# Optimization experiments

Measured on AMD Instinct MI355X. Metric: run time of the kernel, lower is better.

The kernel has to match this reference:

```python
import jax, jax.numpy as jnp
import numpy as np

OUT_FEATURES = 11008
IN_FEATURES = 4096
BLOCK_SIZE = 128
NUM_BLOCKS = IN_FEATURES // BLOCK_SIZE  # 32
M_TOKENS = 4096  # flattened batch*seq


def _pack_int4(q):
    # q: int8 values in [-8, 7], flattened; pack 2 nibbles per int8 (matches pack_int4_to_int8)
    flat = q.reshape(-1)
    u = (flat.astype(jnp.int32) + 8).astype(jnp.uint8)
    packed = (u[0::2] | (u[1::2] << 4)).astype(jnp.int8)
    return packed


def _unpack_int4(packed, shape):
    # matches unpack_int8_to_int4
    pu = packed.astype(jnp.uint8)
    lower = pu & 15
    upper = (pu >> 4) & 15
    un = jnp.stack([lower, upper], axis=1).reshape(-1)
    n = int(np.prod(shape))
    un = un[:n].astype(jnp.int8) - 8
    return un.reshape(shape)


def setup_inputs() -> dict:
    key = jax.random.key(0)
    k_x, k_w, k_b = jax.random.split(key, 3)
    x = jax.random.normal(k_x, (M_TOKENS, IN_FEATURES), dtype=jnp.float32)
    w = jax.random.normal(k_w, (OUT_FEATURES, IN_FEATURES), dtype=jnp.float32) * 0.02
    bias = jax.random.normal(k_b, (OUT_FEATURES,), dtype=jnp.float32) * 0.01
    # blockwise symmetric 4-bit quantization (matches _quantize_blockwise)
    wr = w.reshape(OUT_FEATURES, NUM_BLOCKS, BLOCK_SIZE).transpose(1, 2, 0)  # (nb, bs, out)
    max_val = jnp.max(jnp.abs(wr), axis=1, keepdims=True)  # (nb, 1, out)
    qmax = 7.0
    scale3 = jnp.clip(max_val / qmax, 1e-8, None)
    q = jnp.clip(jnp.round(wr / scale3), -8, 7).astype(jnp.int8)  # (nb, bs, out)
    scale = scale3.squeeze(1)  # (nb, out)
    packed_w = _pack_int4(q)
    return {"x": x, "packed_w": packed_w, "scale": scale, "bias": bias}


def reference(x, packed_w, scale, bias):
    # unpack int4 nibbles -> (num_blocks, block_size, out)
    q = _unpack_int4(packed_w, (NUM_BLOCKS, BLOCK_SIZE, OUT_FEATURES))
    # dequantize with per-(block, out-channel) scale
    w_deq = q.astype(jnp.float32) * scale[:, None, :]  # (nb, bs, out)
    # y = x @ W^T + b, with x blocked along the in dimension
    xb = x.reshape(x.shape[0], NUM_BLOCKS, BLOCK_SIZE)
    y = jnp.einsum('mnb,nbo->mo', xb, w_deq) + bias
    return y
```

## Files before the change

kernel.cpp:

```cpp
#include <hip/hip_runtime.h>
#include <hip/hip_bf16.h>
#include <stdint.h>

#define NOUT 11008
#define KIN  4096
#define MTOK 4096
#define PLD  5504
#define NSTEP 128
#define NTN 43
#define NTM 16
#define ACHUNK 16384
#define BCHUNK 16384
#define WSA_BYTES ((size_t)NTM * NSTEP * ACHUNK)
#define WSW_BYTES ((size_t)NTN * NSTEP * BCHUNK)

typedef short bf16x8 __attribute__((ext_vector_type(8)));
typedef float f32x4  __attribute__((ext_vector_type(4)));

typedef __attribute__((address_space(3))) uint8_t lds_u8_t;
typedef __attribute__((address_space(1))) const uint8_t glb_u8_t;

__device__ __forceinline__ uint32_t bfpack(float lo, float hi){
    __hip_bfloat16 a = __float2bfloat16(lo);
    __hip_bfloat16 b = __float2bfloat16(hi);
    uint16_t ua, ub;
    __builtin_memcpy(&ua, &a, 2);
    __builtin_memcpy(&ub, &b, 2);
    return (uint32_t)ua | ((uint32_t)ub << 16);
}

__device__ __forceinline__ int swzA(int r){ return ((r >> 1) & 3) << 4; }

__device__ __forceinline__ int imin(int a, int b){ return a < b ? a : b; }

__global__ __launch_bounds__(256)
void prepA(const float* __restrict__ x, uint8_t* __restrict__ wsA)
{
    int gid = blockIdx.x * 256 + threadIdx.x;
    int m  = gid >> 10;
    int k  = (gid & 1023) << 2;
    float4 v = *reinterpret_cast<const float4*>(x + (size_t)m * KIN + k);
    uint32_t lo = bfpack(v.x, v.y), hi = bfpack(v.z, v.w);
    int mt = m >> 8, ml = m & 255, t = k >> 5, kl = k & 31;
    size_t dst = (size_t)(mt * NSTEP + t) * ACHUNK + ml * 64 + ((kl * 2) ^ swzA(ml));
    *reinterpret_cast<uint2*>(wsA + dst) = make_uint2(lo, hi);
}

__global__ __launch_bounds__(256)
void prepW2(const int32_t* __restrict__ pw, const float* __restrict__ sc,
            uint8_t* __restrict__ wsW)
{
    const int t  = blockIdx.x;
    const int nt = blockIdx.y;
    const int c  = threadIdx.x;
    const int col = nt * 256 + c;
    const int np  = col >> 1;
    const uint32_t sh = (uint32_t)(col & 1) * 4;
    const int32_t* p = pw + (size_t)(t * 32) * PLD + np;
    const float s  = sc[(size_t)(t >> 2) * NOUT + col];
    const float m8 = -8.f * s;
    uint8_t* out = wsW + ((size_t)nt * NSTEP + t) * BCHUNK + c * 64;
#pragma unroll
    for (int k8 = 0; k8 < 4; ++k8) {
        uint32_t r[4];
#pragma unroll
        for (int kk = 0; kk < 4; ++kk) {
            uint32_t w0 = (uint32_t)p[(size_t)(k8 * 8 + kk * 2)     * PLD];
            uint32_t w1 = (uint32_t)p[(size_t)(k8 * 8 + kk * 2 + 1) * PLD];
            float f0 = fmaf((float)((w0 >> sh) & 15u), s, m8);
            float f1 = fmaf((float)((w1 >> sh) & 15u), s, m8);
            r[kk] = bfpack(f0, f1);
        }
        *reinterpret_cast<uint4*>(out + ((k8 * 16) ^ swzA(c))) = *reinterpret_cast<uint4*>(r);
    }
}

__global__ __launch_bounds__(512, 1)
void qlin_gemm14(const uint8_t* __restrict__ wsA, const uint8_t* __restrict__ wsW,
                 const float* __restrict__ bias, float* __restrict__ y)
{
    __shared__ __align__(16) uint8_t ldsA[4][ACHUNK];

    const int tid  = threadIdx.x;
    const int lane = tid & 63;
    const int wid  = tid >> 6;
    const int wr = wid >> 2, wc = wid & 3;

    const int lb = (blockIdx.x & 7) * 86 + (blockIdx.x >> 3);
    const int mt = lb / NTN, nt = lb % NTN;
    const int m0 = mt * 256, n0 = nt * 256;

    const int cl = lane & 15;
    const int k8 = lane >> 4;

    int aOff[8];
#pragma unroll
    for (int i = 0; i < 8; ++i) {
        int ml = wr * 128 + i * 16 + cl;
        aOff[i] = ml * 64 + ((k8 * 16) ^ swzA(ml));
    }
    int bOff[4];
#pragma unroll
    for (int j = 0; j < 4; ++j) {
        int cc = wc * 64 + j * 16 + cl;
        bOff[j] = cc * 64 + ((k8 * 16) ^ swzA(cc));
    }

    const uint8_t* wsAbase = wsA + (size_t)mt * NSTEP * ACHUNK;
    const uint8_t* wsWbase = wsW + (size_t)nt * NSTEP * BCHUNK;

    f32x4 acc[8][4];
#pragma unroll
    for (int i = 0; i < 8; ++i)
#pragma unroll
        for (int j = 0; j < 4; ++j)
            acc[i][j] = (f32x4){0.f, 0.f, 0.f, 0.f};

    bf16x8 af[4], BFa[4], BFb[4];

#define STAGE_A(buf, t) do { \
    const uint8_t* g_ = wsAbase + (size_t)(t) * ACHUNK + tid * 16; \
    __builtin_amdgcn_global_load_lds((glb_u8_t*)(g_),        (lds_u8_t*)(&ldsA[buf][tid*16]),        16, 0, 0); \
    __builtin_amdgcn_global_load_lds((glb_u8_t*)(g_ + 8192), (lds_u8_t*)(&ldsA[buf][tid*16 + 8192]), 16, 0, 0); \
} while(0)

#define LOADB(BF, tn) do { \
    const uint8_t* gb_ = wsWbase + (size_t)(tn) * BCHUNK; \
    _Pragma("unroll") \
    for (int j = 0; j < 4; ++j) BF[j] = *reinterpret_cast<const bf16x8*>(gb_ + bOff[j]); \
} while(0)

#define BAR() do { \
    asm volatile("" ::: "memory"); \
    __builtin_amdgcn_s_barrier(); \
    asm volatile("" ::: "memory"); \
} while(0)

#define PH_O(cb, sb, st, BFC, BFN, tn) do { \
    STAGE_A(sb, st); \
    LOADB(BFN, tn); \
    _Pragma("unroll") \
    for (int i = 0; i < 4; ++i) af[i] = *reinterpret_cast<const bf16x8*>(ldsA[cb] + aOff[i]); \
    BAR(); \
    __builtin_amdgcn_s_setprio(1); \
    _Pragma("unroll") \
    for (int j = 0; j < 4; ++j) { _Pragma("unroll") \
        for (int i = 0; i < 4; ++i) \
            acc[i][j] = __builtin_amdgcn_mfma_f32_16x16x32_bf16(af[i], BFC[j], acc[i][j], 0, 0, 0); } \
    __builtin_amdgcn_s_setprio(0); \
    BAR(); \
} while(0)

#define PH_E(cb, BFC) do { \
    _Pragma("unroll") \
    for (int i = 0; i < 4; ++i) af[i] = *reinterpret_cast<const bf16x8*>(ldsA[cb] + aOff[4 + i]); \
    BAR(); \
    __builtin_amdgcn_s_setprio(1); \
    _Pragma("unroll") \
    for (int j = 0; j < 4; ++j) { _Pragma("unroll") \
        for (int i = 0; i < 4; ++i) \
            acc[4 + i][j] = __builtin_amdgcn_mfma_f32_16x16x32_bf16(af[i], BFC[j], acc[4 + i][j], 0, 0, 0); } \
    __builtin_amdgcn_s_setprio(0); \
    asm volatile("s_waitcnt vmcnt(12)" ::: "memory"); \
    __builtin_amdgcn_sched_barrier(0); \
    BAR(); \
} while(0)

    STAGE_A(0, 0);
    STAGE_A(1, 1);
    STAGE_A(2, 2);
    LOADB(BFa, 0);
    asm volatile("s_waitcnt vmcnt(8)" ::: "memory");
    __builtin_amdgcn_sched_barrier(0);
    BAR();

#pragma unroll 1
    for (int tb = 0; tb < NSTEP; tb += 4) {
        { const int st = imin(tb + 3, 127), tn = imin(tb + 1, 127);
          PH_O(0, 3, st, BFa, BFb, tn);  PH_E(0, BFa); }
        { const int st = imin(tb + 4, 127), tn = imin(tb + 2, 127);
          PH_O(1, 0, st, BFb, BFa, tn);  PH_E(1, BFb); }
        { const int st = imin(tb + 5, 127), tn = imin(tb + 3, 127);
          PH_O(2, 1, st, BFa, BFb, tn);  PH_E(2, BFa); }
        { const int st = imin(tb + 6, 127), tn = imin(tb + 4, 127);
          PH_O(3, 2, st, BFb, BFa, tn);  PH_E(3, BFb); }
    }

    float bv[4];
#pragma unroll
    for (int j = 0; j < 4; ++j) bv[j] = bias[n0 + wc * 64 + j * 16 + cl];
    const int rg = (lane >> 4) * 4;
#pragma unroll
    for (int i = 0; i < 8; ++i) {
        const int mrow = m0 + wr * 128 + i * 16 + rg;
#pragma unroll
        for (int r = 0; r < 4; ++r) {
            float* yp = y + (size_t)(mrow + r) * NOUT + n0 + wc * 64 + cl;
#pragma unroll
            for (int j = 0; j < 4; ++j)
                yp[j * 16] = acc[i][j][r] + bv[j];
        }
    }

#undef STAGE_A
#undef LOADB
#undef BAR
#undef PH_O
#undef PH_E
}

extern "C" void kernel_launch(void* const* d_in, const int* in_sizes, int n_in,
                              void* d_out, int out_size, void* d_ws, size_t ws_size,
                              hipStream_t stream)
{
    const float*   xin  = (const float*)d_in[0];
    const int32_t* pw   = (const int32_t*)d_in[1];
    const float*   scal = (const float*)d_in[2];
    const float*   bias = (const float*)d_in[3];
    float* y = (float*)d_out;

    uint8_t* wsA = (uint8_t*)d_ws;
    uint8_t* wsW = wsA + WSA_BYTES;

    prepA<<<dim3((MTOK * (KIN / 4)) / 256), 256, 0, stream>>>(xin, wsA);
    prepW2<<<dim3(NSTEP, NTN), 256, 0, stream>>>(pw, scal, wsW);
    qlin_gemm14<<<dim3(NTM * NTN), 512, 0, stream>>>(wsA, wsW, bias, y);
}
```

Measured before the change: 477.9 us.

## Double K-step depth and stage B tiles through LDS instead of direct global loads

Each pipeline step now covers 64 K elements (32 KB chunks) instead of 32, halving the number of steps and barriers. The weight tile is now staged into LDS through asynchronous global_load_lds double-buffering, where before each wave loaded B fragments straight from global memory into registers. The prep kernels change their workspace layouts to match. The intent is to cut barrier and step overhead and to hide B-load latency. In exchange, LDS use rises to 160 KB and the pipeline moves to triple-buffered A with a new waitcnt schedule, which risks stalls or occupancy limits.

```diff
diff --git a/kernel.cpp b/kernel.cpp
--- a/kernel.cpp
+++ b/kernel.cpp
@@ -6,13 +6,13 @@
 #define KIN  4096
 #define MTOK 4096
 #define PLD  5504
-#define NSTEP 128
+#define NSTEP 64
 #define NTN 43
 #define NTM 16
-#define ACHUNK 16384
-#define BCHUNK 16384
-#define WSA_BYTES ((size_t)NTM * NSTEP * ACHUNK)
-#define WSW_BYTES ((size_t)NTN * NSTEP * BCHUNK)
+#define ACH 32768
+#define BCH 32768
+#define WSA_BYTES ((size_t)NTM * NSTEP * ACH)
+#define WSW_BYTES ((size_t)NTN * NSTEP * BCH)
 
 typedef short bf16x8 __attribute__((ext_vector_type(8)));
 typedef float f32x4  __attribute__((ext_vector_type(4)));
@@ -31,8 +31,6 @@
 
 __device__ __forceinline__ int swzA(int r){ return ((r >> 1) & 3) << 4; }
 
-__device__ __forceinline__ int imin(int a, int b){ return a < b ? a : b; }
-
 __global__ __launch_bounds__(256)
 void prepA(const float* __restrict__ x, uint8_t* __restrict__ wsA)
 {
@@ -41,8 +39,8 @@
     int k  = (gid & 1023) << 2;
     float4 v = *reinterpret_cast<const float4*>(x + (size_t)m * KIN + k);
     uint32_t lo = bfpack(v.x, v.y), hi = bfpack(v.z, v.w);
-    int mt = m >> 8, ml = m & 255, t = k >> 5, kl = k & 31;
-    size_t dst = (size_t)(mt * NSTEP + t) * ACHUNK + ml * 64 + ((kl * 2) ^ swzA(ml));
+    int mt = m >> 8, ml = m & 255, t = k >> 6, kh = (k >> 5) & 1, kl = k & 31;
+    size_t dst = (size_t)(mt * NSTEP + t) * ACH + ml * 128 + kh * 64 + ((kl * 2) ^ swzA(ml));
     *reinterpret_cast<uint2*>(wsA + dst) = make_uint2(lo, hi);
 }
 
@@ -56,12 +54,12 @@
     const int col = nt * 256 + c;
     const int np  = col >> 1;
     const uint32_t sh = (uint32_t)(col & 1) * 4;
-    const int32_t* p = pw + (size_t)(t * 32) * PLD + np;
-    const float s  = sc[(size_t)(t >> 2) * NOUT + col];
+    const int32_t* p = pw + (size_t)(t * 64) * PLD + np;
+    const float s  = sc[(size_t)(t >> 1) * NOUT + col];
     const float m8 = -8.f * s;
-    uint8_t* out = wsW + ((size_t)nt * NSTEP + t) * BCHUNK + c * 64;
-#pragma unroll
-    for (int k8 = 0; k8 < 4; ++k8) {
+    uint8_t* out = wsW + ((size_t)nt * NSTEP + t) * BCH + c * 128;
+#pragma unroll
+    for (int k8 = 0; k8 < 8; ++k8) {
         uint32_t r[4];
 #pragma unroll
         for (int kk = 0; kk < 4; ++kk) {
@@ -71,15 +69,17 @@
             float f1 = fmaf((float)((w1 >> sh) & 15u), s, m8);
             r[kk] = bfpack(f0, f1);
         }
-        *reinterpret_cast<uint4*>(out + ((k8 * 16) ^ swzA(c))) = *reinterpret_cast<uint4*>(r);
+        *reinterpret_cast<uint4*>(out + (k8 >> 2) * 64 + (((k8 & 3) * 16) ^ swzA(c)))
+            = *reinterpret_cast<uint4*>(r);
     }
 }
 
 __global__ __launch_bounds__(512, 1)
-void qlin_gemm14(const uint8_t* __restrict__ wsA, const uint8_t* __restrict__ wsW,
+void qlin_gemm15(const uint8_t* __restrict__ wsA, const uint8_t* __restrict__ wsW,
                  const float* __restrict__ bias, float* __restrict__ y)
 {
-    __shared__ __align__(16) uint8_t ldsA[4][ACHUNK];
+    __shared__ __align__(16) uint8_t ldsA[3][ACH];
+    __shared__ __align__(16) uint8_t ldsB[2][BCH];
 
     const int tid  = threadIdx.x;
     const int lane = tid & 63;
@@ -97,17 +97,17 @@
 #pragma unroll
     for (int i = 0; i < 8; ++i) {
         int ml = wr * 128 + i * 16 + cl;
-        aOff[i] = ml * 64 + ((k8 * 16) ^ swzA(ml));
+        aOff[i] = ml * 128 + ((k8 * 16) ^ swzA(ml));
     }
     int bOff[4];
 #pragma unroll
     for (int j = 0; j < 4; ++j) {
         int cc = wc * 64 + j * 16 + cl;
-        bOff[j] = cc * 64 + ((k8 * 16) ^ swzA(cc));
-    }
-
-    const uint8_t* wsAbase = wsA + (size_t)mt * NSTEP * ACHUNK;
-    const uint8_t* wsWbase = wsW + (size_t)nt * NSTEP * BCHUNK;
+        bOff[j] = cc * 128 + ((k8 * 16) ^ swzA(cc));
+    }
+
+    const uint8_t* wsAbase = wsA + (size_t)mt * NSTEP * ACH;
+    const uint8_t* wsWbase = wsW + (size_t)nt * NSTEP * BCH;
 
     f32x4 acc[8][4];
 #pragma unroll
@@ -116,18 +116,22 @@
         for (int j = 0; j < 4; ++j)
             acc[i][j] = (f32x4){0.f, 0.f, 0.f, 0.f};
 
-    bf16x8 af[4], BFa[4], BFb[4];
+    bf16x8 af[4], bf2[4][2];
 
 #define STAGE_A(buf, t) do { \
-    const uint8_t* g_ = wsAbase + (size_t)(t) * ACHUNK + tid * 16; \
-    __builtin_amdgcn_global_load_lds((glb_u8_t*)(g_),        (lds_u8_t*)(&ldsA[buf][tid*16]),        16, 0, 0); \
-    __builtin_amdgcn_global_load_lds((glb_u8_t*)(g_ + 8192), (lds_u8_t*)(&ldsA[buf][tid*16 + 8192]), 16, 0, 0); \
-} while(0)
-
-#define LOADB(BF, tn) do { \
-    const uint8_t* gb_ = wsWbase + (size_t)(tn) * BCHUNK; \
-    _Pragma("unroll") \
-    for (int j = 0; j < 4; ++j) BF[j] = *reinterpret_cast<const bf16x8*>(gb_ + bOff[j]); \
+    const uint8_t* g_ = wsAbase + (size_t)(t) * ACH + tid * 16; \
+    __builtin_amdgcn_global_load_lds((glb_u8_t*)(g_),         (lds_u8_t*)(&ldsA[buf][tid*16]),         16, 0, 0); \
+    __builtin_amdgcn_global_load_lds((glb_u8_t*)(g_ + 8192),  (lds_u8_t*)(&ldsA[buf][tid*16 + 8192]),  16, 0, 0); \
+    __builtin_amdgcn_global_load_lds((glb_u8_t*)(g_ + 16384), (lds_u8_t*)(&ldsA[buf][tid*16 + 16384]), 16, 0, 0); \
+    __builtin_amdgcn_global_load_lds((glb_u8_t*)(g_ + 24576), (lds_u8_t*)(&ldsA[buf][tid*16 + 24576]), 16, 0, 0); \
+} while(0)
+
+#define STAGE_B(buf, t) do { \
+    const uint8_t* g_ = wsWbase + (size_t)(t) * BCH + tid * 16; \
+    __builtin_amdgcn_global_load_lds((glb_u8_t*)(g_),         (lds_u8_t*)(&ldsB[buf][tid*16]),         16, 0, 0); \
+    __builtin_amdgcn_global_load_lds((glb_u8_t*)(g_ + 8192),  (lds_u8_t*)(&ldsB[buf][tid*16 + 8192]),  16, 0, 0); \
+    __builtin_amdgcn_global_load_lds((glb_u8_t*)(g_ + 16384), (lds_u8_t*)(&ldsB[buf][tid*16 + 16384]), 16, 0, 0); \
+    __builtin_amdgcn_global_load_lds((glb_u8_t*)(g_ + 24576), (lds_u8_t*)(&ldsB[buf][tid*16 + 24576]), 16, 0, 0); \
 } while(0)
 
 #define BAR() do { \
@@ -136,55 +140,65 @@
     asm volatile("" ::: "memory"); \
 } while(0)
 
-#define PH_O(cb, sb, st, BFC, BFN, tn) do { \
-    STAGE_A(sb, st); \
-    LOADB(BFN, tn); \
-    _Pragma("unroll") \
-    for (int i = 0; i < 4; ++i) af[i] = *reinterpret_cast<const bf16x8*>(ldsA[cb] + aOff[i]); \
-    BAR(); \
+#define MFMA16(IBASE, H) do { \
     __builtin_amdgcn_s_setprio(1); \
     _Pragma("unroll") \
     for (int j = 0; j < 4; ++j) { _Pragma("unroll") \
         for (int i = 0; i < 4; ++i) \
-            acc[i][j] = __builtin_amdgcn_mfma_f32_16x16x32_bf16(af[i], BFC[j], acc[i][j], 0, 0, 0); } \
+            acc[(IBASE) + i][j] = __builtin_amdgcn_mfma_f32_16x16x32_bf16(af[i], bf2[j][H], acc[(IBASE) + i][j], 0, 0, 0); } \
     __builtin_amdgcn_s_setprio(0); \
-    BAR(); \
-} while(0)
-
-#define PH_E(cb, BFC) do { \
-    _Pragma("unroll") \
-    for (int i = 0; i < 4; ++i) af[i] = *reinterpret_cast<const bf16x8*>(ldsA[cb] + aOff[4 + i]); \
-    BAR(); \
-    __builtin_amdgcn_s_setprio(1); \
-    _Pragma("unroll") \
-    for (int j = 0; j < 4; ++j) { _Pragma("unroll") \
-        for (int i = 0; i < 4; ++i) \
-            acc[4 + i][j] = __builtin_amdgcn_mfma_f32_16x16x32_bf16(af[i], BFC[j], acc[4 + i][j], 0, 0, 0); } \
-    __builtin_amdgcn_s_setprio(0); \
-    asm volatile("s_waitcnt vmcnt(12)" ::: "memory"); \
+} while(0)
+
+#define PH_O(cbA, cbB, sbB, tB) do { \
+    STAGE_B(sbB, tB); \
+    _Pragma("unroll") \
+    for (int j = 0; j < 4; ++j) bf2[j][0] = *reinterpret_cast<const bf16x8*>(ldsB[cbB] + bOff[j]); \
+    _Pragma("unroll") \
+    for (int i = 0; i < 4; ++i) af[i] = *reinterpret_cast<const bf16x8*>(ldsA[cbA] + aOff[i]); \
+    BAR(); \
+    MFMA16(0, 0); \
+    _Pragma("unroll") \
+    for (int j = 0; j < 4; ++j) bf2[j][1] = *reinterpret_cast<const bf16x8*>(ldsB[cbB] + bOff[j] + 64); \
+    _Pragma("unroll") \
+    for (int i = 0; i < 4; ++i) af[i] = *reinterpret_cast<const bf16x8*>(ldsA[cbA] + aOff[i] + 64); \
+    MFMA16(0, 1); \
+    BAR(); \
+} while(0)
+
+#define PH_E(cbA, sbA, tA) do { \
+    STAGE_A(sbA, tA); \
+    _Pragma("unroll") \
+    for (int i = 0; i < 4; ++i) af[i] = *reinterpret_cast<const bf16x8*>(ldsA[cbA] + aOff[4 + i]); \
+    BAR(); \
+    MFMA16(4, 0); \
+    _Pragma("unroll") \
+    for (int i = 0; i < 4; ++i) af[i] = *reinterpret_cast<const bf16x8*>(ldsA[cbA] + aOff[4 + i] + 64); \
+    MFMA16(4, 1); \
+    asm volatile("s_waitcnt vmcnt(4)" ::: "memory"); \
     __builtin_amdgcn_sched_barrier(0); \
     BAR(); \
 } while(0)
 
     STAGE_A(0, 0);
+    STAGE_B(0, 0);
     STAGE_A(1, 1);
-    STAGE_A(2, 2);
-    LOADB(BFa, 0);
-    asm volatile("s_waitcnt vmcnt(8)" ::: "memory");
+    asm volatile("s_waitcnt vmcnt(4)" ::: "memory");
     __builtin_amdgcn_sched_barrier(0);
     BAR();
 
 #pragma unroll 1
-    for (int tb = 0; tb < NSTEP; tb += 4) {
-        { const int st = imin(tb + 3, 127), tn = imin(tb + 1, 127);
-          PH_O(0, 3, st, BFa, BFb, tn);  PH_E(0, BFa); }
-        { const int st = imin(tb + 4, 127), tn = imin(tb + 2, 127);
-          PH_O(1, 0, st, BFb, BFa, tn);  PH_E(1, BFb); }
-        { const int st = imin(tb + 5, 127), tn = imin(tb + 3, 127);
-          PH_O(2, 1, st, BFa, BFb, tn);  PH_E(2, BFa); }
-        { const int st = imin(tb + 6, 127), tn = imin(tb + 4, 127);
-          PH_O(3, 2, st, BFb, BFa, tn);  PH_E(3, BFb); }
-    }
+    for (int tb = 0; tb < 60; tb += 6) {
+        PH_O(0, 0, 1, tb + 1);  PH_E(0, 2, tb + 2);
+        PH_O(1, 1, 0, tb + 2);  PH_E(1, 0, tb + 3);
+        PH_O(2, 0, 1, tb + 3);  PH_E(2, 1, tb + 4);
+        PH_O(0, 1, 0, tb + 4);  PH_E(0, 2, tb + 5);
+        PH_O(1, 0, 1, tb + 5);  PH_E(1, 0, tb + 6);
+        PH_O(2, 1, 0, tb + 6);  PH_E(2, 1, tb + 7);
+    }
+    PH_O(0, 0, 1, 61);  PH_E(0, 2, 62);
+    PH_O(1, 1, 0, 62);  PH_E(1, 0, 63);
+    PH_O(2, 0, 1, 63);  PH_E(2, 1, 63);
+    PH_O(0, 1, 0, 63);  PH_E(0, 2, 63);
 
     float bv[4];
 #pragma unroll
@@ -203,8 +217,9 @@
     }
 
 #undef STAGE_A
-#undef LOADB
+#undef STAGE_B
 #undef BAR
+#undef MFMA16
 #undef PH_O
 #undef PH_E
 }
@@ -224,5 +239,5 @@
 
     prepA<<<dim3((MTOK * (KIN / 4)) / 256), 256, 0, stream>>>(xin, wsA);
     prepW2<<<dim3(NSTEP, NTN), 256, 0, stream>>>(pw, scal, wsW);
-    qlin_gemm14<<<dim3(NTM * NTN), 512, 0, stream>>>(wsA, wsW, bias, y);
-}
+    qlin_gemm15<<<dim3(NTM * NTN), 512, 0, stream>>>(wsA, wsW, bias, y);
+}
```

New measurement: 526.1 us. 10.1% more time.
